# Kernel optimization log

Hardware: AMD Instinct MI355X
Metric: run time of the kernel (lower is better)

Reference implementation:

```python
import jax, jax.numpy as jnp
import numpy as np

N, F, D, H, L = 1536, 6, 64, 4, 2
DH = D // H
FF = 4 * D
EPS = 1e-5

def setup_inputs() -> dict:
    key = jax.random.key(0)
    ks = iter(jax.random.split(key, 32))
    def g(shape, scale=0.05):
        return jax.random.normal(next(ks), shape, jnp.float32) * scale
    return dict(
        node_feats=g((N, F), 1.0),
        proj_w=g((D, F)), proj_b=g((D,)),
        in_w=g((L, 3 * D, D)), in_b=g((L, 3 * D)),
        out_w=g((L, D, D)), out_b=g((L, D)),
        ff1_w=g((L, FF, D)), ff1_b=g((L, FF)),
        ff2_w=g((L, D, FF)), ff2_b=g((L, D)),
        ln1_g=jnp.ones((L, D), jnp.float32), ln1_b=jnp.zeros((L, D), jnp.float32),
        ln2_g=jnp.ones((L, D), jnp.float32), ln2_b=jnp.zeros((L, D), jnp.float32),
        ns_w=g((1, D)), ns_b=g((1,)),
        e1_w=g((D, 2 * D)), e1_b=g((D,)),
        e2_w=g((1, D)), e2_b=g((1,)),
    )

def _layernorm(x, g, b):
    mu = x.mean(-1, keepdims=True)
    var = ((x - mu) ** 2).mean(-1, keepdims=True)
    return (x - mu) / jnp.sqrt(var + EPS) * g + b

def _forward(node_feats, proj_w, proj_b, in_w, in_b, out_w, out_b,
             ff1_w, ff1_b, ff2_w, ff2_b, ln1_g, ln1_b, ln2_g, ln2_b,
             ns_w, ns_b, e1_w, e1_b, e2_w, e2_b):
    x = node_feats @ proj_w.T + proj_b  # (N, D)
    # Transformer encoder, post-norm, eval mode (dropout off); seq_len=N, batch=1.
    for l in range(L):
        qkv = x @ in_w[l].T + in_b[l]  # (N, 3D)
        q, k, v = jnp.split(qkv, 3, axis=-1)
        q = q.reshape(N, H, DH).transpose(1, 0, 2)  # (H, N, DH)
        k = k.reshape(N, H, DH).transpose(1, 0, 2)
        v = v.reshape(N, H, DH).transpose(1, 0, 2)
        scores = jnp.einsum('hnd,hmd->hnm', q, k) / jnp.sqrt(jnp.float32(DH))
        attn = jax.nn.softmax(scores, axis=-1)
        o = jnp.einsum('hnm,hmd->hnd', attn, v).transpose(1, 0, 2).reshape(N, D)
        sa = o @ out_w[l].T + out_b[l]
        x = _layernorm(x + sa, ln1_g[l], ln1_b[l])
        ff = jax.nn.relu(x @ ff1_w[l].T + ff1_b[l]) @ ff2_w[l].T + ff2_b[l]
        x = _layernorm(x + ff, ln2_g[l], ln2_b[l])
    node_logits = (x @ ns_w.T + ns_b)[:, 0]  # (N,)
    # Edge scoring: Linear(2D->D) on concat[x_i, x_j] == x_i @ A^T + x_j @ B^T + b1.
    # Precompute the two projections to avoid materializing the (N, N, 2D) concat.
    A, B = e1_w[:, :D], e1_w[:, D:]
    u = x @ A.T  # (N, D)
    w = x @ B.T  # (N, D)
    h = jax.nn.relu(u[:, None, :] + w[None, :, :] + e1_b)  # (N, N, D)
    edge_logits = jnp.einsum('nmd,d->nm', h, e2_w[0]) + e2_b[0]
    return node_logits, edge_logits

def reference(node_feats, proj_w, proj_b, in_w, in_b, out_w, out_b,
              ff1_w, ff1_b, ff2_w, ff2_b, ln1_g, ln1_b, ln2_g, ln2_b,
              ns_w, ns_b, e1_w, e1_b, e2_w, e2_b):
    return _forward(node_feats, proj_w, proj_b, in_w, in_b, out_w, out_b,
                    ff1_w, ff1_b, ff2_w, ff2_b, ln1_g, ln1_b, ln2_g, ln2_b,
                    ns_w, ns_b, e1_w, e1_b, e2_w, e2_b)
```

## Files before the change

### kernel.cpp

```cpp
#include <hip/hip_runtime.h>
#include <hip/hip_bf16.h>

#define N 1536
#define F 6
#define D 64
#define H 4
#define DH 16
#define FFDIM 256
#define NL 2
#define EPS 1e-5f
#define KS 16
#define KB (N / KS)
#define KW (KB / 4)
#define QB 128
#define NPART KS

static __device__ __forceinline__ float dot4(float4 a, float4 b) {
    return a.x * b.x + a.y * b.y + a.z * b.z + a.w * b.w;
}

union SmA {
    float sinw[48][D];
    struct { float k[KB][DH]; float v[KB][DH]; } kv;
    float rd[4][QB][DH + 1];
};
__global__ __launch_bounds__(256) void k_attn0(const float* __restrict__ nf,
                                               const float* __restrict__ pw,
                                               const float* __restrict__ pb,
                                               const float* __restrict__ iw,
                                               const float* __restrict__ ib,
                                               float* __restrict__ x,
                                               float* __restrict__ accp,
                                               float* __restrict__ psump) {
    __shared__ __align__(16) SmA sm;
    __shared__ float pwl[D * F];
    __shared__ float pbl[D];
    __shared__ float nfk[KB * F];
    __shared__ float nfq[QB * F];
    __shared__ float eff[48][F];
    __shared__ float beff[48];
    int ks = blockIdx.x, qc = blockIdx.y, h = blockIdx.z;
    int t = threadIdx.x;
    int wv = t >> 6, lane = t & 63;

    for (int i = t; i < D * F; i += 256) pwl[i] = pw[i];
    if (t < D) pbl[t] = pb[t];
    for (int i = t; i < KB * F; i += 256) nfk[i] = nf[ks * KB * F + i];
    for (int i = t; i < QB * F; i += 256) nfq[i] = nf[qc * QB * F + i];
    for (int i = t; i < 48 * D; i += 256) {
        int oo = i >> 6, e = i & 63;
        int o = (oo < 16) ? (h * DH + oo)
              : (oo < 32) ? (D + h * DH + (oo - 16))
                          : (2 * D + h * DH + (oo - 32));
        sm.sinw[oo][e] = iw[o * D + e];
    }
    __syncthreads();

    for (int i = t; i < 48 * F; i += 256) {
        int oo = i / F, fx = i % F;
        float a = 0.f;
#pragma unroll 8
        for (int e = 0; e < D; ++e) a += sm.sinw[oo][e] * pwl[e * F + fx];
        eff[oo][fx] = a;
    }
    if (t < 48) {
        int o = (t < 16) ? (h * DH + t)
              : (t < 32) ? (D + h * DH + (t - 16))
                         : (2 * D + h * DH + (t - 32));
        float a = ib[o];
#pragma unroll 8
        for (int e = 0; e < D; ++e) a += sm.sinw[t][e] * pbl[e];
        beff[t] = a;
    }
    __syncthreads();

    {
        int i = t & 31, rg = t >> 5;
        int oo = (i < 16) ? (16 + i) : (32 + (i - 16));
        float w0 = eff[oo][0], w1 = eff[oo][1], w2 = eff[oo][2];
        float w3 = eff[oo][3], w4 = eff[oo][4], w5 = eff[oo][5];
        float bo = beff[oo];
        for (int r = rg * (KB / 8); r < (rg + 1) * (KB / 8); ++r) {
            const float* nr = &nfk[r * F];
            float val = bo + nr[0] * w0 + nr[1] * w1 + nr[2] * w2
                           + nr[3] * w3 + nr[4] * w4 + nr[5] * w5;
            if (i < 16) sm.kv.k[r][i] = val;
            else        sm.kv.v[r][i - 16] = val;
        }
    }
    float q[2][DH];
#pragma unroll
    for (int j = 0; j < 2; ++j) {
        const float* nr = &nfq[(j * 64 + lane) * F];
        float n0 = nr[0], n1 = nr[1], n2 = nr[2], n3 = nr[3], n4 = nr[4], n5 = nr[5];
#pragma unroll
        for (int i = 0; i < DH; ++i)
            q[j][i] = 0.25f * (beff[i] + n0 * eff[i][0] + n1 * eff[i][1] + n2 * eff[i][2]
                                       + n3 * eff[i][3] + n4 * eff[i][4] + n5 * eff[i][5]);
    }
    if (ks == 0 && h == 0) {
        for (int i = t; i < QB * D; i += 256) {
            int row = i >> 6, e = i & 63;
            const float* nr = &nfq[row * F];
            float a = pbl[e];
#pragma unroll
            for (int f = 0; f < F; ++f) a += nr[f] * pwl[e * F + f];
            x[(qc * QB + row) * D + e] = a;
        }
    }
    __syncthreads();

    float acc[2][DH];
#pragma unroll
    for (int j = 0; j < 2; ++j)
#pragma unroll
        for (int i = 0; i < DH; ++i) acc[j][i] = 0.f;
    float psum[2] = {0.f, 0.f};

#pragma unroll 2
    for (int jk = 0; jk < KW; ++jk) {
        int r = wv * KW + jk;
        float4 k0 = *(const float4*)&sm.kv.k[r][0];
        float4 k1 = *(const float4*)&sm.kv.k[r][4];
        float4 k2 = *(const float4*)&sm.kv.k[r][8];
        float4 k3 = *(const float4*)&sm.kv.k[r][12];
        float p[2];
#pragma unroll
        for (int j = 0; j < 2; ++j) {
            float s = q[j][0] * k0.x + q[j][1] * k0.y + q[j][2] * k0.z + q[j][3] * k0.w
                    + q[j][4] * k1.x + q[j][5] * k1.y + q[j][6] * k1.z + q[j][7] * k1.w
                    + q[j][8] * k2.x + q[j][9] * k2.y + q[j][10] * k2.z + q[j][11] * k2.w
                    + q[j][12] * k3.x + q[j][13] * k3.y + q[j][14] * k3.z + q[j][15] * k3.w;
            p[j] = __expf(s);
            psum[j] += p[j];
        }
        float4 v0 = *(const float4*)&sm.kv.v[r][0];
        float4 v1 = *(const float4*)&sm.kv.v[r][4];
        float4 v2 = *(const float4*)&sm.kv.v[r][8];
        float4 v3 = *(const float4*)&sm.kv.v[r][12];
#pragma unroll
        for (int j = 0; j < 2; ++j) {
            acc[j][0] += p[j] * v0.x;  acc[j][1] += p[j] * v0.y;
            acc[j][2] += p[j] * v0.z;  acc[j][3] += p[j] * v0.w;
            acc[j][4] += p[j] * v1.x;  acc[j][5] += p[j] * v1.y;
            acc[j][6] += p[j] * v1.z;  acc[j][7] += p[j] * v1.w;
            acc[j][8] += p[j] * v2.x;  acc[j][9] += p[j] * v2.y;
            acc[j][10] += p[j] * v2.z; acc[j][11] += p[j] * v2.w;
            acc[j][12] += p[j] * v3.x; acc[j][13] += p[j] * v3.y;
            acc[j][14] += p[j] * v3.z; acc[j][15] += p[j] * v3.w;
        }
    }

    __syncthreads();
#pragma unroll
    for (int j = 0; j < 2; ++j) {
        int qq = j * 64 + lane;
#pragma unroll
        for (int i = 0; i < DH; ++i) sm.rd[wv][qq][i] = acc[j][i];
        sm.rd[wv][qq][DH] = psum[j];
    }
    __syncthreads();

    for (int i = t; i < QB * (DH + 1); i += 256) {
        int qq = i / (DH + 1), c = i % (DH + 1);
        float s = sm.rd[0][qq][c] + sm.rd[1][qq][c] + sm.rd[2][qq][c] + sm.rd[3][qq][c];
        int n = qc * QB + qq;
        if (c < DH)
            accp[((size_t)ks * N + n) * D + h * DH + c] = s;
        else
            psump[((size_t)ks * N + n) * H + h] = s;
    }
}

struct SmemKV { float k[KB][DH]; float v[KB][DH]; };
__global__ __launch_bounds__(256) void k_attn_part(const float* __restrict__ qkv,
                                                   float* __restrict__ accp,
                                                   float* __restrict__ psump) {
    __shared__ __align__(16) union {
        SmemKV kv;
        float rd[4][QB][DH + 1];
    } sm;
    int ks = blockIdx.x, qc = blockIdx.y, h = blockIdx.z;
    int t = threadIdx.x;
    int wv = t >> 6, lane = t & 63;

    for (int i = t; i < KB * 4; i += 256) {
        int row = i >> 2, c4 = (i & 3) * 4;
        const float* base = qkv + (size_t)(ks * KB + row) * (3 * D) + D + h * DH + c4;
        *(float4*)&sm.kv.k[row][c4] = *(const float4*)base;
        *(float4*)&sm.kv.v[row][c4] = *(const float4*)(base + D);
    }

    float q[2][DH];
#pragma unroll
    for (int j = 0; j < 2; ++j) {
        const float4* qp =
            (const float4*)(qkv + (size_t)(qc * QB + j * 64 + lane) * (3 * D) + h * DH);
#pragma unroll
        for (int e = 0; e < 4; ++e) {
            float4 v = qp[e];
            q[j][e * 4 + 0] = v.x * 0.25f;
            q[j][e * 4 + 1] = v.y * 0.25f;
            q[j][e * 4 + 2] = v.z * 0.25f;
            q[j][e * 4 + 3] = v.w * 0.25f;
        }
    }
    __syncthreads();

    float acc[2][DH];
#pragma unroll
    for (int j = 0; j < 2; ++j)
#pragma unroll
        for (int i = 0; i < DH; ++i) acc[j][i] = 0.f;
    float psum[2] = {0.f, 0.f};

#pragma unroll 2
    for (int jk = 0; jk < KW; ++jk) {
        int r = wv * KW + jk;
        float4 k0 = *(const float4*)&sm.kv.k[r][0];
        float4 k1 = *(const float4*)&sm.kv.k[r][4];
        float4 k2 = *(const float4*)&sm.kv.k[r][8];
        float4 k3 = *(const float4*)&sm.kv.k[r][12];
        float p[2];
#pragma unroll
        for (int j = 0; j < 2; ++j) {
            float s = q[j][0] * k0.x + q[j][1] * k0.y + q[j][2] * k0.z + q[j][3] * k0.w
                    + q[j][4] * k1.x + q[j][5] * k1.y + q[j][6] * k1.z + q[j][7] * k1.w
                    + q[j][8] * k2.x + q[j][9] * k2.y + q[j][10] * k2.z + q[j][11] * k2.w
                    + q[j][12] * k3.x + q[j][13] * k3.y + q[j][14] * k3.z + q[j][15] * k3.w;
            p[j] = __expf(s);
            psum[j] += p[j];
        }
        float4 v0 = *(const float4*)&sm.kv.v[r][0];
        float4 v1 = *(const float4*)&sm.kv.v[r][4];
        float4 v2 = *(const float4*)&sm.kv.v[r][8];
        float4 v3 = *(const float4*)&sm.kv.v[r][12];
#pragma unroll
        for (int j = 0; j < 2; ++j) {
            acc[j][0] += p[j] * v0.x;  acc[j][1] += p[j] * v0.y;
            acc[j][2] += p[j] * v0.z;  acc[j][3] += p[j] * v0.w;
            acc[j][4] += p[j] * v1.x;  acc[j][5] += p[j] * v1.y;
            acc[j][6] += p[j] * v1.z;  acc[j][7] += p[j] * v1.w;
            acc[j][8] += p[j] * v2.x;  acc[j][9] += p[j] * v2.y;
            acc[j][10] += p[j] * v2.z; acc[j][11] += p[j] * v2.w;
            acc[j][12] += p[j] * v3.x; acc[j][13] += p[j] * v3.y;
            acc[j][14] += p[j] * v3.z; acc[j][15] += p[j] * v3.w;
        }
    }

    __syncthreads();
#pragma unroll
    for (int j = 0; j < 2; ++j) {
        int qq = j * 64 + lane;
#pragma unroll
        for (int i = 0; i < DH; ++i) sm.rd[wv][qq][i] = acc[j][i];
        sm.rd[wv][qq][DH] = psum[j];
    }
    __syncthreads();

    for (int i = t; i < QB * (DH + 1); i += 256) {
        int qq = i / (DH + 1), c = i % (DH + 1);
        float s = sm.rd[0][qq][c] + sm.rd[1][qq][c] + sm.rd[2][qq][c] + sm.rd[3][qq][c];
        int n = qc * QB + qq;
        if (c < DH)
            accp[((size_t)ks * N + n) * D + h * DH + c] = s;
        else
            psump[((size_t)ks * N + n) * H + h] = s;
    }
}

__global__ __launch_bounds__(256) void k_attn_ffn(const float* __restrict__ accp,
                                                  const float* __restrict__ psump,
                                                  const float* __restrict__ ow,
                                                  const float* __restrict__ ob,
                                                  const float* __restrict__ g1,
                                                  const float* __restrict__ be1,
                                                  const float* __restrict__ w1,
                                                  const float* __restrict__ b1,
                                                  const float* __restrict__ w2,
                                                  const float* __restrict__ b2,
                                                  const float* __restrict__ g2,
                                                  const float* __restrict__ be2,
                                                  float* __restrict__ x,
                                                  const float* __restrict__ nw,
                                                  const float* __restrict__ nb,
                                                  float* __restrict__ nqkv,
                                                  int tail,
                                                  const float* __restrict__ nsw,
                                                  const float* __restrict__ nsb,
                                                  const float* __restrict__ e1w,
                                                  const float* __restrict__ e1b,
                                                  float* __restrict__ nodeo,
                                                  float* __restrict__ u,
                                                  float* __restrict__ wbuf) {
    __shared__ __align__(16) float so[4][D];
    __shared__ __align__(16) float sx[4][D];
    __shared__ __align__(16) float sh[4][FFDIM];
    __shared__ float sp[4][4][D];
    int t = threadIdx.x;
    int r = t >> 6, e = t & 63;
    int n = blockIdx.x * 4 + r;

    {
        float a = 0.f, p = 0.f;
#pragma unroll 8
        for (int pp = 0; pp < NPART; ++pp) {
            a += accp[((size_t)pp * N + n) * D + e];
            p += psump[((size_t)pp * N + n) * H + (e >> 4)];
        }
        so[r][e] = a / p;
    }
    __syncthreads();

    {
        const float4* ir = (const float4*)so[r];
        const float4* wr = (const float4*)(ow + e * D);
        float acc = ob[e];
#pragma unroll
        for (int k = 0; k < D / 4; ++k) acc += dot4(ir[k], wr[k]);
        float y = x[n * D + e] + acc;
        float mu = y;
#pragma unroll
        for (int off = 32; off; off >>= 1) mu += __shfl_xor(mu, off, 64);
        mu *= (1.f / 64.f);
        float diff = y - mu;
        float var = diff * diff;
#pragma unroll
        for (int off = 32; off; off >>= 1) var += __shfl_xor(var, off, 64);
        var *= (1.f / 64.f);
        sx[r][e] = diff * rsqrtf(var + EPS) * g1[e] + be1[e];
    }
    __syncthreads();

    {
        const float4* wr = (const float4*)(w1 + t * D);
        float acc[4];
        float bb = b1[t];
#pragma unroll
        for (int rr = 0; rr < 4; ++rr) acc[rr] = bb;
#pragma unroll
        for (int k = 0; k < D / 4; ++k) {
            float4 wv = wr[k];
#pragma unroll
            for (int rr = 0; rr < 4; ++rr) acc[rr] += dot4(wv, *(const float4*)&sx[rr][k * 4]);
        }
#pragma unroll
        for (int rr = 0; rr < 4; ++rr) sh[rr][t] = fmaxf(acc[rr], 0.f);
    }
    __syncthreads();

    {
        int d = t & 63, c = t >> 6;
        const float4* wr = (const float4*)(w2 + d * FFDIM + c * 64);
        float acc[4] = {0.f, 0.f, 0.f, 0.f};
#pragma unroll
        for (int k = 0; k < 16; ++k) {
            float4 wv = wr[k];
#pragma unroll
            for (int rr = 0; rr < 4; ++rr)
                acc[rr] += dot4(wv, *(const float4*)&sh[rr][c * 64 + k * 4]);
        }
#pragma unroll
        for (int rr = 0; rr < 4; ++rr) sp[rr][c][d] = acc[rr];
    }
    __syncthreads();

    {
        float y = sx[r][e] + b2[e] + sp[r][0][e] + sp[r][1][e] + sp[r][2][e] + sp[r][3][e];
        float mu = y;
#pragma unroll
        for (int off = 32; off; off >>= 1) mu += __shfl_xor(mu, off, 64);
        mu *= (1.f / 64.f);
        float diff = y - mu;
        float var = diff * diff;
#pragma unroll
        for (int off = 32; off; off >>= 1) var += __shfl_xor(var, off, 64);
        var *= (1.f / 64.f);
        float xv = diff * rsqrtf(var + EPS) * g2[e] + be2[e];
        x[n * D + e] = xv;
        sx[r][e] = xv;
    }

    if (nqkv) {
        __syncthreads();
        if (t < 3 * D) {
            const float4* wr = (const float4*)(nw + t * D);
            float bb = nb[t];
            float a0 = bb, a1 = bb, a2 = bb, a3 = bb;
#pragma unroll
            for (int k = 0; k < D / 4; ++k) {
                float4 wv = wr[k];
                a0 += dot4(wv, *(const float4*)&sx[0][k * 4]);
                a1 += dot4(wv, *(const float4*)&sx[1][k * 4]);
                a2 += dot4(wv, *(const float4*)&sx[2][k * 4]);
                a3 += dot4(wv, *(const float4*)&sx[3][k * 4]);
            }
            int n0 = blockIdx.x * 4;
            nqkv[(n0 + 0) * (3 * D) + t] = a0;
            nqkv[(n0 + 1) * (3 * D) + t] = a1;
            nqkv[(n0 + 2) * (3 * D) + t] = a2;
            nqkv[(n0 + 3) * (3 * D) + t] = a3;
        }
    }

    if (!tail) return;
    __syncthreads();

    {
        const float4* xr = (const float4*)sx[r];
        const float4* ar = (const float4*)(e1w + e * 2 * D);
        const float4* br = (const float4*)(e1w + e * 2 * D + D);
        float au = 0.f, aw = 0.f;
#pragma unroll
        for (int k = 0; k < D / 4; ++k) {
            float4 xv = xr[k], av = ar[k], bv = br[k];
            au += dot4(xv, av);
            aw += dot4(xv, bv);
        }
        u[n * D + e] = au + e1b[e];
        wbuf[n * D + e] = aw;
        float p = sx[r][e] * nsw[e];
#pragma unroll
        for (int off = 32; off; off >>= 1) p += __shfl_xor(p, off, 64);
        if (e == 0) nodeo[n] = p + nsb[0];
    }
}

__global__ __launch_bounds__(256) void k_edge(const float* __restrict__ u,
                                              const float* __restrict__ w,
                                              const float* __restrict__ e2w,
                                              const float* __restrict__ e2b,
                                              float* __restrict__ out) {
    __shared__ __align__(16) float su[64][68];
    __shared__ __align__(16) float sw[64][68];
    __shared__ __align__(16) float sv[64];
    int tn = blockIdx.y * 64, tm = blockIdx.x * 64;
    int t = threadIdx.x;
    for (int i = t; i < 64 * 16; i += 256) {
        int r = i >> 4, c4 = (i & 15) * 4;
        *(float4*)&su[r][c4] = *(const float4*)&u[(tn + r) * D + c4];
        *(float4*)&sw[r][c4] = *(const float4*)&w[(tm + r) * D + c4];
    }
    if (t < 64) sv[t] = e2w[t];
    __syncthreads();
    float eb = e2b[0];
    int c0 = t & 15, r0 = t >> 4;

    float acc[4][4];
#pragma unroll
    for (int j = 0; j < 4; ++j)
#pragma unroll
        for (int k = 0; k < 4; ++k) acc[j][k] = 0.f;

#pragma unroll 4
    for (int e0 = 0; e0 < 64; e0 += 4) {
        float4 vv = *(const float4*)&sv[e0];
        float4 a[4], bb[4];
#pragma unroll
        for (int j = 0; j < 4; ++j) a[j] = *(const float4*)&su[r0 + 16 * j][e0];
#pragma unroll
        for (int k = 0; k < 4; ++k) bb[k] = *(const float4*)&sw[c0 + 16 * k][e0];
#pragma unroll
        for (int j = 0; j < 4; ++j)
#pragma unroll
            for (int k = 0; k < 4; ++k) {
                acc[j][k] += fmaxf(a[j].x + bb[k].x, 0.f) * vv.x;
                acc[j][k] += fmaxf(a[j].y + bb[k].y, 0.f) * vv.y;
                acc[j][k] += fmaxf(a[j].z + bb[k].z, 0.f) * vv.z;
                acc[j][k] += fmaxf(a[j].w + bb[k].w, 0.f) * vv.w;
            }
    }
#pragma unroll
    for (int j = 0; j < 4; ++j)
#pragma unroll
        for (int k = 0; k < 4; ++k)
            out[(size_t)(tn + r0 + 16 * j) * N + (tm + c0 + 16 * k)] = acc[j][k] + eb;
}

extern "C" void kernel_launch(void* const* d_in, const int* in_sizes, int n_in,
                              void* d_out, int out_size, void* d_ws, size_t ws_size,
                              hipStream_t stream) {
    const float* node_feats = (const float*)d_in[0];
    const float* proj_w = (const float*)d_in[1];
    const float* proj_b = (const float*)d_in[2];
    const float* in_w = (const float*)d_in[3];
    const float* in_b = (const float*)d_in[4];
    const float* out_w = (const float*)d_in[5];
    const float* out_b = (const float*)d_in[6];
    const float* ff1_w = (const float*)d_in[7];
    const float* ff1_b = (const float*)d_in[8];
    const float* ff2_w = (const float*)d_in[9];
    const float* ff2_b = (const float*)d_in[10];
    const float* ln1_g = (const float*)d_in[11];
    const float* ln1_b = (const float*)d_in[12];
    const float* ln2_g = (const float*)d_in[13];
    const float* ln2_b = (const float*)d_in[14];
    const float* ns_w = (const float*)d_in[15];
    const float* ns_b = (const float*)d_in[16];
    const float* e1_w = (const float*)d_in[17];
    const float* e1_b = (const float*)d_in[18];
    const float* e2_w = (const float*)d_in[19];
    const float* e2_b = (const float*)d_in[20];

    float* out = (float*)d_out;

    float* x = (float*)d_ws;
    float* qkv = x + N * D;
    float* accp = qkv + N * 3 * D;
    float* psump = accp + (size_t)NPART * N * D;
    float* u = psump + (size_t)NPART * N * H;
    float* wbuf = u + N * D;

    dim3 agrid(KS, N / QB, H);

    k_attn0<<<agrid, 256, 0, stream>>>(node_feats, proj_w, proj_b,
                                       in_w, in_b, x, accp, psump);
    k_attn_ffn<<<N / 4, 256, 0, stream>>>(
        accp, psump, out_w, out_b, ln1_g, ln1_b,
        ff1_w, ff1_b, ff2_w, ff2_b, ln2_g, ln2_b, x,
        in_w + (size_t)3 * D * D, in_b + 3 * D, qkv,
        0, nullptr, nullptr, nullptr, nullptr, nullptr, nullptr, nullptr);
    k_attn_part<<<agrid, 256, 0, stream>>>(qkv, accp, psump);
    k_attn_ffn<<<N / 4, 256, 0, stream>>>(
        accp, psump, out_w + (size_t)D * D, out_b + D,
        ln1_g + D, ln1_b + D,
        ff1_w + (size_t)FFDIM * D, ff1_b + FFDIM,
        ff2_w + (size_t)D * FFDIM, ff2_b + D,
        ln2_g + D, ln2_b + D, x,
        nullptr, nullptr, nullptr,
        1, ns_w, ns_b, e1_w, e1_b, out, u, wbuf);
    {
        dim3 grid(N / 64, N / 64);
        k_edge<<<grid, 256, 0, stream>>>(u, wbuf, e2_w, e2_b, out + N);
    }
}
```

Measured before the change: 111.3 us.

## Halve key splits and double attention block size to eight waves

Changes the attention split-K decomposition from 16 key partitions with 4 waves per block to 8 key partitions with 8 waves (512 threads) per block. The cross-wave reduction gets a two-phase shared-memory pass: waves 0-3 write, then waves 4-7 accumulate. This halves the partial buffers written and later summed by the FFN kernel, but the grid has half as many blocks and each block carries extra sync and register pressure. The partial-sum loop in the consumer is fully unrolled.

```diff
diff --git a/kernel.cpp b/kernel.cpp
--- a/kernel.cpp
+++ b/kernel.cpp
@@ -9,9 +9,10 @@
 #define FFDIM 256
 #define NL 2
 #define EPS 1e-5f
-#define KS 16
+#define KS 8
 #define KB (N / KS)
-#define KW (KB / 4)
+#define NW 8
+#define KW (KB / NW)
 #define QB 128
 #define NPART KS
 
@@ -24,7 +25,7 @@
     struct { float k[KB][DH]; float v[KB][DH]; } kv;
     float rd[4][QB][DH + 1];
 };
-__global__ __launch_bounds__(256) void k_attn0(const float* __restrict__ nf,
+__global__ __launch_bounds__(512) void k_attn0(const float* __restrict__ nf,
                                                const float* __restrict__ pw,
                                                const float* __restrict__ pb,
                                                const float* __restrict__ iw,
@@ -43,11 +44,11 @@
     int t = threadIdx.x;
     int wv = t >> 6, lane = t & 63;
 
-    for (int i = t; i < D * F; i += 256) pwl[i] = pw[i];
+    for (int i = t; i < D * F; i += 512) pwl[i] = pw[i];
     if (t < D) pbl[t] = pb[t];
-    for (int i = t; i < KB * F; i += 256) nfk[i] = nf[ks * KB * F + i];
-    for (int i = t; i < QB * F; i += 256) nfq[i] = nf[qc * QB * F + i];
-    for (int i = t; i < 48 * D; i += 256) {
+    for (int i = t; i < KB * F; i += 512) nfk[i] = nf[ks * KB * F + i];
+    for (int i = t; i < QB * F; i += 512) nfq[i] = nf[qc * QB * F + i];
+    for (int i = t; i < 48 * D; i += 512) {
         int oo = i >> 6, e = i & 63;
         int o = (oo < 16) ? (h * DH + oo)
               : (oo < 32) ? (D + h * DH + (oo - 16))
@@ -56,7 +57,7 @@
     }
     __syncthreads();
 
-    for (int i = t; i < 48 * F; i += 256) {
+    for (int i = t; i < 48 * F; i += 512) {
         int oo = i / F, fx = i % F;
         float a = 0.f;
 #pragma unroll 8
@@ -80,7 +81,7 @@
         float w0 = eff[oo][0], w1 = eff[oo][1], w2 = eff[oo][2];
         float w3 = eff[oo][3], w4 = eff[oo][4], w5 = eff[oo][5];
         float bo = beff[oo];
-        for (int r = rg * (KB / 8); r < (rg + 1) * (KB / 8); ++r) {
+        for (int r = rg * (KB / 16); r < (rg + 1) * (KB / 16); ++r) {
             const float* nr = &nfk[r * F];
             float val = bo + nr[0] * w0 + nr[1] * w1 + nr[2] * w2
                            + nr[3] * w3 + nr[4] * w4 + nr[5] * w5;
@@ -99,7 +100,7 @@
                                        + n3 * eff[i][3] + n4 * eff[i][4] + n5 * eff[i][5]);
     }
     if (ks == 0 && h == 0) {
-        for (int i = t; i < QB * D; i += 256) {
+        for (int i = t; i < QB * D; i += 512) {
             int row = i >> 6, e = i & 63;
             const float* nr = &nfq[row * F];
             float a = pbl[e];
@@ -152,16 +153,29 @@
     }
 
     __syncthreads();
-#pragma unroll
-    for (int j = 0; j < 2; ++j) {
-        int qq = j * 64 + lane;
-#pragma unroll
-        for (int i = 0; i < DH; ++i) sm.rd[wv][qq][i] = acc[j][i];
-        sm.rd[wv][qq][DH] = psum[j];
-    }
-    __syncthreads();
-
-    for (int i = t; i < QB * (DH + 1); i += 256) {
+    if (wv < 4) {
+#pragma unroll
+        for (int j = 0; j < 2; ++j) {
+            int qq = j * 64 + lane;
+#pragma unroll
+            for (int i = 0; i < DH; ++i) sm.rd[wv][qq][i] = acc[j][i];
+            sm.rd[wv][qq][DH] = psum[j];
+        }
+    }
+    __syncthreads();
+    if (wv >= 4) {
+        int w2 = wv - 4;
+#pragma unroll
+        for (int j = 0; j < 2; ++j) {
+            int qq = j * 64 + lane;
+#pragma unroll
+            for (int i = 0; i < DH; ++i) sm.rd[w2][qq][i] += acc[j][i];
+            sm.rd[w2][qq][DH] += psum[j];
+        }
+    }
+    __syncthreads();
+
+    for (int i = t; i < QB * (DH + 1); i += 512) {
         int qq = i / (DH + 1), c = i % (DH + 1);
         float s = sm.rd[0][qq][c] + sm.rd[1][qq][c] + sm.rd[2][qq][c] + sm.rd[3][qq][c];
         int n = qc * QB + qq;
@@ -173,7 +187,7 @@
 }
 
 struct SmemKV { float k[KB][DH]; float v[KB][DH]; };
-__global__ __launch_bounds__(256) void k_attn_part(const float* __restrict__ qkv,
+__global__ __launch_bounds__(512) void k_attn_part(const float* __restrict__ qkv,
                                                    float* __restrict__ accp,
                                                    float* __restrict__ psump) {
     __shared__ __align__(16) union {
@@ -184,7 +198,7 @@
     int t = threadIdx.x;
     int wv = t >> 6, lane = t & 63;
 
-    for (int i = t; i < KB * 4; i += 256) {
+    for (int i = t; i < KB * 4; i += 512) {
         int row = i >> 2, c4 = (i & 3) * 4;
         const float* base = qkv + (size_t)(ks * KB + row) * (3 * D) + D + h * DH + c4;
         *(float4*)&sm.kv.k[row][c4] = *(const float4*)base;
@@ -249,16 +263,29 @@
     }
 
     __syncthreads();
-#pragma unroll
-    for (int j = 0; j < 2; ++j) {
-        int qq = j * 64 + lane;
-#pragma unroll
-        for (int i = 0; i < DH; ++i) sm.rd[wv][qq][i] = acc[j][i];
-        sm.rd[wv][qq][DH] = psum[j];
-    }
-    __syncthreads();
-
-    for (int i = t; i < QB * (DH + 1); i += 256) {
+    if (wv < 4) {
+#pragma unroll
+        for (int j = 0; j < 2; ++j) {
+            int qq = j * 64 + lane;
+#pragma unroll
+            for (int i = 0; i < DH; ++i) sm.rd[wv][qq][i] = acc[j][i];
+            sm.rd[wv][qq][DH] = psum[j];
+        }
+    }
+    __syncthreads();
+    if (wv >= 4) {
+        int w2 = wv - 4;
+#pragma unroll
+        for (int j = 0; j < 2; ++j) {
+            int qq = j * 64 + lane;
+#pragma unroll
+            for (int i = 0; i < DH; ++i) sm.rd[w2][qq][i] += acc[j][i];
+            sm.rd[w2][qq][DH] += psum[j];
+        }
+    }
+    __syncthreads();
+
+    for (int i = t; i < QB * (DH + 1); i += 512) {
         int qq = i / (DH + 1), c = i % (DH + 1);
         float s = sm.rd[0][qq][c] + sm.rd[1][qq][c] + sm.rd[2][qq][c] + sm.rd[3][qq][c];
         int n = qc * QB + qq;
@@ -303,7 +330,7 @@
 
     {
         float a = 0.f, p = 0.f;
-#pragma unroll 8
+#pragma unroll
         for (int pp = 0; pp < NPART; ++pp) {
             a += accp[((size_t)pp * N + n) * D + e];
             p += psump[((size_t)pp * N + n) * H + (e >> 4)];
@@ -513,14 +540,14 @@
 
     dim3 agrid(KS, N / QB, H);
 
-    k_attn0<<<agrid, 256, 0, stream>>>(node_feats, proj_w, proj_b,
+    k_attn0<<<agrid, 512, 0, stream>>>(node_feats, proj_w, proj_b,
                                        in_w, in_b, x, accp, psump);
     k_attn_ffn<<<N / 4, 256, 0, stream>>>(
         accp, psump, out_w, out_b, ln1_g, ln1_b,
         ff1_w, ff1_b, ff2_w, ff2_b, ln2_g, ln2_b, x,
         in_w + (size_t)3 * D * D, in_b + 3 * D, qkv,
         0, nullptr, nullptr, nullptr, nullptr, nullptr, nullptr, nullptr);
-    k_attn_part<<<agrid, 256, 0, stream>>>(qkv, accp, psump);
+    k_attn_part<<<agrid, 512, 0, stream>>>(qkv, accp, psump);
     k_attn_ffn<<<N / 4, 256, 0, stream>>>(
         accp, psump, out_w + (size_t)D * D, out_b + D,
         ln1_g + D, ln1_b + D,
```

After: 108.6 us. 2.4% less time.
